# Performance work log

Measured on AMD Instinct MI355X. Metric: run time of the kernel, lower is better.

The kernel has to match this reference:

```python
import math
import jax, jax.numpy as jnp
import numpy as np

FACTOR = 5

def setup_inputs() -> dict:
    key = jax.random.key(0)
    kq, kk, kv, ki = jax.random.split(key, 4)
    b, h, L, d = 4, 8, 4096, 64
    sample_k = min(L, int(FACTOR * math.log(L + 1)))  # 41
    q = jax.random.normal(kq, (b, h, L, d), dtype=jnp.float32)
    k = jax.random.normal(kk, (b, h, L, d), dtype=jnp.float32)
    v = jax.random.normal(kv, (b, h, L, d), dtype=jnp.float32)
    index_sample = jax.random.randint(ki, (L, sample_k), 0, L, dtype=jnp.int64)
    return {"q": q, "k": k, "v": v, "index_sample": index_sample}

def reference(q, k, v, index_sample):
    b, h, l_q, d = q.shape
    l_k = k.shape[2]
    n_top = min(l_q, int(FACTOR * math.log(l_q + 1)))
    # --- ProbSparse query selection ---
    # k_sample[b,h,q,s,d] = k[b,h,index_sample[q,s],d]  (avoids the O(lq*lk*d) expand)
    k_sample = k[:, :, index_sample, :]                      # (b,h,l_q,sample_k,d)
    qk_sample = jnp.einsum('bhqd,bhqsd->bhqs', q, k_sample)  # (b,h,l_q,sample_k)
    m = qk_sample.max(axis=-1) - qk_sample.mean(axis=-1)     # sparsity measure
    _, top_q = jax.lax.top_k(m, n_top)                       # (b,h,n_top)
    # --- sparse attention on selected queries ---
    q_reduce = jnp.take_along_axis(q, top_q[..., None], axis=2)  # (b,h,n_top,d)
    scale = 1.0 / math.sqrt(d)
    scores = jnp.einsum('bhnd,bhkd->bhnk', q_reduce, k) * scale
    attn = jax.nn.softmax(scores, axis=-1)
    context_top = jnp.einsum('bhnk,bhkd->bhnd', attn, v)
    # --- scatter into mean-initialized context (attn_mask is None path) ---
    context = jnp.broadcast_to(v.mean(axis=2, keepdims=True), (b, h, l_q, d))
    bi = jnp.arange(b)[:, None, None]
    hi = jnp.arange(h)[None, :, None]
    context = context.at[bi, hi, top_q].set(context_top)
    return context
```

## Files before the change

### kernel.cpp

```cpp
#include <hip/hip_runtime.h>
#include <hip/hip_bf16.h>


#define NTOP 41
#define NPAD 48
#define TILES 8
#define TL 512
#define CH 64
#define NCHUNK (TL / CH)
#define CAND_CAP 64

typedef __attribute__((ext_vector_type(8))) short bf16x8;
typedef __attribute__((ext_vector_type(4))) float f32x4;

__device__ __forceinline__ unsigned short f2bf(float f) {
    unsigned int x = __float_as_uint(f);
    unsigned int r = (x + 0x7FFFu + ((x >> 16) & 1u)) >> 16;
    return (unsigned short)r;
}
__device__ __forceinline__ unsigned int pack2(float lo, float hi) {
    return ((unsigned int)f2bf(hi) << 16) | f2bf(lo);
}

__global__ __launch_bounds__(256) void kA_scores(const float* __restrict__ q,
                                                 const float* __restrict__ k,
                                                 const int* __restrict__ idxs,
                                                 float* __restrict__ m_out) {
    int t = threadIdx.x;
    int lane = t & 63, w = t >> 6;
    int g = lane >> 3, sl = lane & 7;
    int lb = ((blockIdx.x & 7) << 9) + (blockIdx.x >> 3);
    long long qflat = (long long)lb * 32 + w * 8 + g;
    int bh = (int)(qflat >> 12);
    int qi = (int)(qflat & 4095);
    const float4* q4 = (const float4*)q;
    const float4* k4 = (const float4*)k;
    float4 qa = q4[qflat * 16 + sl * 2];
    float4 qb = q4[qflat * 16 + sl * 2 + 1];
    const int* irow = idxs + qi * 41;
    long long kbase = ((long long)bh << 12) * 16;
    float maxv = -1e30f, sum = 0.f;
    for (int s = 0; s < 41; s++) {
        int ki = irow[s] & 4095;
        float4 ka = k4[kbase + (long long)ki * 16 + sl * 2];
        float4 kb = k4[kbase + (long long)ki * 16 + sl * 2 + 1];
        float p = 0.f;
        p = fmaf(qa.x, ka.x, p); p = fmaf(qa.y, ka.y, p);
        p = fmaf(qa.z, ka.z, p); p = fmaf(qa.w, ka.w, p);
        p = fmaf(qb.x, kb.x, p); p = fmaf(qb.y, kb.y, p);
        p = fmaf(qb.z, kb.z, p); p = fmaf(qb.w, kb.w, p);
        p += __shfl_xor(p, 1);
        p += __shfl_xor(p, 2);
        p += __shfl_xor(p, 4);
        maxv = fmaxf(maxv, p);
        sum += p;
    }
    if (sl == 0) m_out[qflat] = maxv - sum * (1.0f / 41.0f);
}

__global__ __launch_bounds__(256) void kB_topk(const float* __restrict__ m_in,
                                               int* __restrict__ topq) {
    __shared__ unsigned int uvals[4096];
    __shared__ unsigned int hist[256];
    __shared__ unsigned int scal[4];
    __shared__ int candIdx[CAND_CAP];
    __shared__ unsigned int candU[CAND_CAP];
    int bh = blockIdx.x, t = threadIdx.x;
    for (int i = t; i < 4096; i += 256) {
        unsigned int b = __float_as_uint(m_in[bh * 4096 + i]);
        uvals[i] = (b & 0x80000000u) ? ~b : (b | 0x80000000u);
    }
    hist[t] = 0;
    __syncthreads();
    for (int i = t; i < 4096; i += 256) atomicAdd(&hist[uvals[i] >> 24], 1u);
    __syncthreads();
    if (t == 0) {
        unsigned int cum = 0, b1 = 0, ca = 0;
        for (int j = 255; j >= 0; j--) {
            if (cum + hist[j] >= 41u) { b1 = (unsigned)j; ca = cum; break; }
            cum += hist[j];
        }
        scal[0] = b1; scal[1] = ca;
    }
    __syncthreads();
    unsigned int b1 = scal[0];
    hist[t] = 0;
    __syncthreads();
    for (int i = t; i < 4096; i += 256)
        if ((uvals[i] >> 24) == b1) atomicAdd(&hist[(uvals[i] >> 16) & 255u], 1u);
    __syncthreads();
    if (t == 0) {
        unsigned int cum = scal[1], b2 = 0;
        for (int j = 255; j >= 0; j--) {
            if (cum + hist[j] >= 41u) { b2 = (unsigned)j; break; }
            cum += hist[j];
        }
        scal[2] = (b1 << 24) | (b2 << 16);
        scal[3] = 0;
    }
    __syncthreads();
    unsigned int T = scal[2];
    for (int i = t; i < 4096; i += 256) {
        unsigned int u = uvals[i];
        if (u >= T) {
            unsigned int pos = atomicAdd(&scal[3], 1u);
            if (pos < CAND_CAP) { candIdx[pos] = i; candU[pos] = u; }
        }
    }
    __syncthreads();
    if (t < 64) {
        int n = (int)min(scal[3], (unsigned)CAND_CAP);
        unsigned int myU = (t < n) ? candU[t] : 0u;
        int myI = (t < n) ? candIdx[t] : 0x7fffffff;
        for (int it = 0; it < NTOP; it++) {
            unsigned int bu = myU;
            int bi = myI;
            for (int off = 32; off; off >>= 1) {
                unsigned int ou = __shfl_xor(bu, off);
                int oi = __shfl_xor(bi, off);
                if (ou > bu || (ou == bu && oi < bi)) { bu = ou; bi = oi; }
            }
            if (t == 0) topq[bh * NTOP + it] = bi;
            if (myI == bi) { myU = 0u; myI = 0x7fffffff; }
        }
    }
}

__global__ __launch_bounds__(256) void kC1(const float* __restrict__ v,
                                           float* __restrict__ vpart) {
    int bh = blockIdx.x, chn = blockIdx.y, t = threadIdx.x;
    int d = t & 63, r = t >> 6;
    long long base = ((long long)bh << 12) + chn * 256;
    float acc = 0.f;
    for (int i = 0; i < 64; i++) acc += v[(base + i * 4 + r) * 64 + d];
    __shared__ float red[256];
    red[t] = acc;
    __syncthreads();
    if (r == 0) vpart[(bh * 16 + chn) * 64 + d] = red[d] + red[64 + d] + red[128 + d] + red[192 + d];
}

__global__ void kC2(const float* __restrict__ vpart, float* __restrict__ vmean) {
    int bh = blockIdx.x, d = threadIdx.x;
    float s = 0.f;
#pragma unroll
    for (int c = 0; c < 16; c++) s += vpart[(bh * 16 + c) * 64 + d];
    vmean[bh * 64 + d] = s * (1.0f / 4096.0f);
}

__global__ __launch_bounds__(256) void kD(const float* __restrict__ vmean,
                                          float* __restrict__ out) {
    long long g0 = (long long)blockIdx.x * 1024 + threadIdx.x;
    float4* out4 = (float4*)out;
#pragma unroll
    for (int i = 0; i < 4; i++) {
        long long g = g0 + i * 256;
        int bh = (int)(g >> 16);
        int d4 = (int)(g & 15);
        out4[g] = *(const float4*)(vmean + bh * 64 + d4 * 4);
    }
}

__global__ __launch_bounds__(256) void kE_attn(const float* __restrict__ q,
                                               const float* __restrict__ k,
                                               const float* __restrict__ v,
                                               const int* __restrict__ topq,
                                               float* __restrict__ part) {
    __shared__ unsigned short qs[NPAD * 72];
    __shared__ unsigned short kb[CH * 72];
    __shared__ unsigned short vt[64 * 72];
    __shared__ unsigned short pb[NPAD * 72];
    __shared__ float sp[NPAD * 65];
    __shared__ float m_i[NPAD], l_i[NPAD], fac[NPAD];

    const int t = threadIdx.x;
    const int tile = blockIdx.x, bh = blockIdx.y;
    const int lane = t & 63, w = t >> 6;
    const int c = lane & 15, quad = lane >> 4;
    const long long bhbase = ((long long)bh) << 12;

    const float4* q4f = (const float4*)q;
    const float4* k4f = (const float4*)k;
    const float4* v4f = (const float4*)v;

    for (int i = t; i < NTOP * 16; i += 256) {
        int n = i >> 4, oc = i & 15;
        int row = topq[bh * NTOP + n];
        float4 val = q4f[(bhbase + row) * 16 + oc];
        uint2 pk;
        pk.x = pack2(val.x * 0.125f, val.y * 0.125f);
        pk.y = pack2(val.z * 0.125f, val.w * 0.125f);
        *(uint2*)(&qs[n * 72 + oc * 4]) = pk;
    }
    for (int i = t; i < 7 * 72; i += 256) {
        qs[NTOP * 72 + i] = 0;
        pb[NTOP * 72 + i] = 0;
    }
    if (t < NPAD) { m_i[t] = -1e30f; l_i[t] = 0.f; fac[t] = 0.f; }

    f32x4 oacc[3];
#pragma unroll
    for (int qt = 0; qt < 3; qt++) oacc[qt] = (f32x4){0.f, 0.f, 0.f, 0.f};

    const int l0 = tile * TL;
    for (int ch = 0; ch < NCHUNK; ch++) {
        const int lb = l0 + ch * CH;
        __syncthreads();
#pragma unroll
        for (int i = 0; i < 4; i++) {
            int idx = i * 256 + t;
            int j = idx >> 4, oc = idx & 15;
            float4 val = k4f[(bhbase + lb + j) * 16 + oc];
            uint2 pk;
            pk.x = pack2(val.x, val.y);
            pk.y = pack2(val.z, val.w);
            *(uint2*)(&kb[j * 72 + oc * 4]) = pk;
        }
        {
            int jp = t & 31, o = t >> 5;
            float4 a0 = v4f[(bhbase + lb + 2 * jp) * 16 + o * 2];
            float4 a1 = v4f[(bhbase + lb + 2 * jp) * 16 + o * 2 + 1];
            float4 b0 = v4f[(bhbase + lb + 2 * jp + 1) * 16 + o * 2];
            float4 b1 = v4f[(bhbase + lb + 2 * jp + 1) * 16 + o * 2 + 1];
            float av[8] = {a0.x, a0.y, a0.z, a0.w, a1.x, a1.y, a1.z, a1.w};
            float bv[8] = {b0.x, b0.y, b0.z, b0.w, b1.x, b1.y, b1.z, b1.w};
#pragma unroll
            for (int e = 0; e < 8; e++)
                *(unsigned int*)(&vt[(o * 8 + e) * 72 + 2 * jp]) = pack2(av[e], bv[e]);
        }
        __syncthreads();
        {
            const bf16x8 bk0 = *(const bf16x8*)(&kb[(w * 16 + c) * 72 + quad * 8]);
            const bf16x8 bk1 = *(const bf16x8*)(&kb[(w * 16 + c) * 72 + quad * 8 + 32]);
#pragma unroll
            for (int qt = 0; qt < 3; qt++) {
                const bf16x8 a0 = *(const bf16x8*)(&qs[(qt * 16 + c) * 72 + quad * 8]);
                const bf16x8 a1 = *(const bf16x8*)(&qs[(qt * 16 + c) * 72 + quad * 8 + 32]);
                f32x4 s4 = (f32x4){0.f, 0.f, 0.f, 0.f};
                s4 = __builtin_amdgcn_mfma_f32_16x16x32_bf16(a0, bk0, s4, 0, 0, 0);
                s4 = __builtin_amdgcn_mfma_f32_16x16x32_bf16(a1, bk1, s4, 0, 0, 0);
#pragma unroll
                for (int r = 0; r < 4; r++)
                    sp[(qt * 16 + quad * 4 + r) * 65 + w * 16 + c] = s4[r];
            }
        }
        __syncthreads();
        if (t < NTOP * 4) {
            int n = t >> 2, sub = t & 3;
            float rm = -1e30f;
#pragma unroll
            for (int j = 0; j < 16; j++) rm = fmaxf(rm, sp[n * 65 + sub * 16 + j]);
            rm = fmaxf(rm, __shfl_xor(rm, 1));
            rm = fmaxf(rm, __shfl_xor(rm, 2));
            float mo = m_i[n];
            float mn = fmaxf(mo, rm);
            float ssum = 0.f;
#pragma unroll
            for (int j = 0; j < 16; j += 2) {
                float e0 = __expf(sp[n * 65 + sub * 16 + j] - mn);
                float e1 = __expf(sp[n * 65 + sub * 16 + j + 1] - mn);
                ssum += e0 + e1;
                *(unsigned int*)(&pb[n * 72 + sub * 16 + j]) = pack2(e0, e1);
            }
            ssum += __shfl_xor(ssum, 1);
            ssum += __shfl_xor(ssum, 2);
            if (sub == 0) {
                float f = __expf(mo - mn);
                fac[n] = f;
                l_i[n] = l_i[n] * f + ssum;
                m_i[n] = mn;
            }
        }
        __syncthreads();
        {
            const bf16x8 bv0 = *(const bf16x8*)(&vt[(w * 16 + c) * 72 + quad * 8]);
            const bf16x8 bv1 = *(const bf16x8*)(&vt[(w * 16 + c) * 72 + quad * 8 + 32]);
#pragma unroll
            for (int qt = 0; qt < 3; qt++) {
                const bf16x8 a0 = *(const bf16x8*)(&pb[(qt * 16 + c) * 72 + quad * 8]);
                const bf16x8 a1 = *(const bf16x8*)(&pb[(qt * 16 + c) * 72 + quad * 8 + 32]);
                f32x4 o = oacc[qt];
                o.x *= fac[qt * 16 + quad * 4 + 0];
                o.y *= fac[qt * 16 + quad * 4 + 1];
                o.z *= fac[qt * 16 + quad * 4 + 2];
                o.w *= fac[qt * 16 + quad * 4 + 3];
                o = __builtin_amdgcn_mfma_f32_16x16x32_bf16(a0, bv0, o, 0, 0, 0);
                o = __builtin_amdgcn_mfma_f32_16x16x32_bf16(a1, bv1, o, 0, 0, 0);
                oacc[qt] = o;
            }
        }
    }
    __syncthreads();
    long long pbase = ((long long)(bh * TILES + tile)) * NTOP * 66;
    if (t < NTOP) {
        part[pbase + t * 66 + 0] = m_i[t];
        part[pbase + t * 66 + 1] = l_i[t];
    }
#pragma unroll
    for (int qt = 0; qt < 3; qt++) {
#pragma unroll
        for (int r = 0; r < 4; r++) {
            int n = qt * 16 + quad * 4 + r;
            if (n < NTOP) part[pbase + (long long)n * 66 + 2 + w * 16 + c] = oacc[qt][r];
        }
    }
}

__global__ __launch_bounds__(256) void kF_combine(const float* __restrict__ part,
                                                  const int* __restrict__ topq,
                                                  float* __restrict__ out) {
    int t = threadIdx.x;
    int bh = blockIdx.x;
    int n = blockIdx.y * 4 + (t >> 6);
    int d = t & 63;
    if (n >= NTOP) return;
    long long base = ((long long)(bh * TILES)) * NTOP * 66 + (long long)n * 66;
    const long long ts = (long long)NTOP * 66;
    float M = -1e30f;
#pragma unroll
    for (int tt = 0; tt < TILES; tt++) M = fmaxf(M, part[base + tt * ts]);
    float L = 0.f, acc = 0.f;
#pragma unroll
    for (int tt = 0; tt < TILES; tt++) {
        float mt = part[base + tt * ts];
        float wgt = __expf(mt - M);
        L += part[base + tt * ts + 1] * wgt;
        acc += part[base + tt * ts + 2 + d] * wgt;
    }
    int row = topq[bh * NTOP + n];
    out[(((long long)bh << 12) + row) * 64 + d] = acc / L;
}

extern "C" void kernel_launch(void* const* d_in, const int* in_sizes, int n_in,
                              void* d_out, int out_size, void* d_ws, size_t ws_size,
                              hipStream_t stream) {
    const float* q = (const float*)d_in[0];
    const float* k = (const float*)d_in[1];
    const float* v = (const float*)d_in[2];
    const int* idxs = (const int*)d_in[3];
    float* out = (float*)d_out;

    char* ws = (char*)d_ws;
    float* ws_m = (float*)ws;
    int* ws_topq = (int*)(ws + 524288);
    float* ws_vpart = (float*)(ws + 532480);
    float* ws_vmean = (float*)(ws + 663552);
    float* ws_part = (float*)(ws + 671744);

    kA_scores<<<4096, 256, 0, stream>>>(q, k, idxs, ws_m);
    kB_topk<<<32, 256, 0, stream>>>(ws_m, ws_topq);
    kC1<<<dim3(32, 16), 256, 0, stream>>>(v, ws_vpart);
    kC2<<<32, 64, 0, stream>>>(ws_vpart, ws_vmean);
    kD<<<2048, 256, 0, stream>>>(ws_vmean, out);
    kE_attn<<<dim3(TILES, 32), 256, 0, stream>>>(q, k, v, ws_topq, ws_part);
    kF_combine<<<dim3(32, 11), 256, 0, stream>>>(ws_part, ws_topq, out);
}
```

Measured before the change: 261.6 us.

## Stage sample indices in LDS, fold vmean into fill, split attention into more tiles

New measurement: 252.1 us. 1.04x faster.

```diff
diff --git a/kernel.cpp b/kernel.cpp
--- a/kernel.cpp
+++ b/kernel.cpp
@@ -4,10 +4,7 @@
 
 #define NTOP 41
 #define NPAD 48
-#define TILES 8
-#define TL 512
 #define CH 64
-#define NCHUNK (TL / CH)
 #define CAND_CAP 64
 
 typedef __attribute__((ext_vector_type(8))) short bf16x8;
@@ -21,37 +18,68 @@
 __device__ __forceinline__ unsigned int pack2(float lo, float hi) {
     return ((unsigned int)f2bf(hi) << 16) | f2bf(lo);
 }
+__device__ __forceinline__ float dot8(const float4& qa, const float4& qb,
+                                      const float4& ka, const float4& kb) {
+    float p = 0.f;
+    p = fmaf(qa.x, ka.x, p); p = fmaf(qa.y, ka.y, p);
+    p = fmaf(qa.z, ka.z, p); p = fmaf(qa.w, ka.w, p);
+    p = fmaf(qb.x, kb.x, p); p = fmaf(qb.y, kb.y, p);
+    p = fmaf(qb.z, kb.z, p); p = fmaf(qb.w, kb.w, p);
+    return p;
+}
+__device__ __forceinline__ float red8(float p) {
+    p += __shfl_xor(p, 1);
+    p += __shfl_xor(p, 2);
+    p += __shfl_xor(p, 4);
+    return p;
+}
 
 __global__ __launch_bounds__(256) void kA_scores(const float* __restrict__ q,
                                                  const float* __restrict__ k,
                                                  const int* __restrict__ idxs,
                                                  float* __restrict__ m_out) {
+    __shared__ int sidx[32 * 41];
     int t = threadIdx.x;
     int lane = t & 63, w = t >> 6;
     int g = lane >> 3, sl = lane & 7;
     int lb = ((blockIdx.x & 7) << 9) + (blockIdx.x >> 3);
     long long qflat = (long long)lb * 32 + w * 8 + g;
     int bh = (int)(qflat >> 12);
-    int qi = (int)(qflat & 4095);
+    int qi0 = (lb * 32) & 4095;
+    for (int i = t; i < 32 * 41; i += 256)
+        sidx[i] = idxs[(long long)qi0 * 41 + i] & 4095;
     const float4* q4 = (const float4*)q;
     const float4* k4 = (const float4*)k;
     float4 qa = q4[qflat * 16 + sl * 2];
     float4 qb = q4[qflat * 16 + sl * 2 + 1];
-    const int* irow = idxs + qi * 41;
     long long kbase = ((long long)bh << 12) * 16;
+    __syncthreads();
+    const int* irow = sidx + (w * 8 + g) * 41;
     float maxv = -1e30f, sum = 0.f;
-    for (int s = 0; s < 41; s++) {
-        int ki = irow[s] & 4095;
+#pragma unroll 2
+    for (int g4 = 0; g4 < 10; g4++) {
+        int ki0 = irow[g4 * 4 + 0], ki1 = irow[g4 * 4 + 1];
+        int ki2 = irow[g4 * 4 + 2], ki3 = irow[g4 * 4 + 3];
+        float4 ka0 = k4[kbase + (long long)ki0 * 16 + sl * 2];
+        float4 kb0 = k4[kbase + (long long)ki0 * 16 + sl * 2 + 1];
+        float4 ka1 = k4[kbase + (long long)ki1 * 16 + sl * 2];
+        float4 kb1 = k4[kbase + (long long)ki1 * 16 + sl * 2 + 1];
+        float4 ka2 = k4[kbase + (long long)ki2 * 16 + sl * 2];
+        float4 kb2 = k4[kbase + (long long)ki2 * 16 + sl * 2 + 1];
+        float4 ka3 = k4[kbase + (long long)ki3 * 16 + sl * 2];
+        float4 kb3 = k4[kbase + (long long)ki3 * 16 + sl * 2 + 1];
+        float p0 = red8(dot8(qa, qb, ka0, kb0));
+        float p1 = red8(dot8(qa, qb, ka1, kb1));
+        float p2 = red8(dot8(qa, qb, ka2, kb2));
+        float p3 = red8(dot8(qa, qb, ka3, kb3));
+        maxv = fmaxf(maxv, fmaxf(fmaxf(p0, p1), fmaxf(p2, p3)));
+        sum += (p0 + p1) + (p2 + p3);
+    }
+    {
+        int ki = irow[40];
         float4 ka = k4[kbase + (long long)ki * 16 + sl * 2];
         float4 kb = k4[kbase + (long long)ki * 16 + sl * 2 + 1];
-        float p = 0.f;
-        p = fmaf(qa.x, ka.x, p); p = fmaf(qa.y, ka.y, p);
-        p = fmaf(qa.z, ka.z, p); p = fmaf(qa.w, ka.w, p);
-        p = fmaf(qb.x, kb.x, p); p = fmaf(qb.y, kb.y, p);
-        p = fmaf(qb.z, kb.z, p); p = fmaf(qb.w, kb.w, p);
-        p += __shfl_xor(p, 1);
-        p += __shfl_xor(p, 2);
-        p += __shfl_xor(p, 4);
+        float p = red8(dot8(qa, qb, ka, kb));
         maxv = fmaxf(maxv, p);
         sum += p;
     }
@@ -139,24 +167,25 @@
     if (r == 0) vpart[(bh * 16 + chn) * 64 + d] = red[d] + red[64 + d] + red[128 + d] + red[192 + d];
 }
 
-__global__ void kC2(const float* __restrict__ vpart, float* __restrict__ vmean) {
-    int bh = blockIdx.x, d = threadIdx.x;
-    float s = 0.f;
-#pragma unroll
-    for (int c = 0; c < 16; c++) s += vpart[(bh * 16 + c) * 64 + d];
-    vmean[bh * 64 + d] = s * (1.0f / 4096.0f);
-}
-
-__global__ __launch_bounds__(256) void kD(const float* __restrict__ vmean,
+__global__ __launch_bounds__(256) void kD(const float* __restrict__ vpart,
                                           float* __restrict__ out) {
-    long long g0 = (long long)blockIdx.x * 1024 + threadIdx.x;
+    __shared__ __align__(16) float vm[64];
+    int t = threadIdx.x;
+    int bh = blockIdx.x >> 6;
+    if (t < 64) {
+        float s = 0.f;
+#pragma unroll
+        for (int c = 0; c < 16; c++) s += vpart[(bh * 16 + c) * 64 + t];
+        vm[t] = s * (1.0f / 4096.0f);
+    }
+    __syncthreads();
+    long long g0 = (long long)blockIdx.x * 1024 + t;
     float4* out4 = (float4*)out;
 #pragma unroll
     for (int i = 0; i < 4; i++) {
-        long long g = g0 + i * 256;
-        int bh = (int)(g >> 16);
-        int d4 = (int)(g & 15);
-        out4[g] = *(const float4*)(vmean + bh * 64 + d4 * 4);
+        long long gg = g0 + i * 256;
+        int d4 = (int)(gg & 15);
+        out4[gg] = *(const float4*)(&vm[d4 * 4]);
     }
 }
 
@@ -164,7 +193,7 @@
                                                const float* __restrict__ k,
                                                const float* __restrict__ v,
                                                const int* __restrict__ topq,
-                                               float* __restrict__ part) {
+                                               float* __restrict__ part, int tl) {
     __shared__ unsigned short qs[NPAD * 72];
     __shared__ unsigned short kb[CH * 72];
     __shared__ unsigned short vt[64 * 72];
@@ -174,6 +203,7 @@
 
     const int t = threadIdx.x;
     const int tile = blockIdx.x, bh = blockIdx.y;
+    const int tiles = gridDim.x;
     const int lane = t & 63, w = t >> 6;
     const int c = lane & 15, quad = lane >> 4;
     const long long bhbase = ((long long)bh) << 12;
@@ -201,8 +231,9 @@
 #pragma unroll
     for (int qt = 0; qt < 3; qt++) oacc[qt] = (f32x4){0.f, 0.f, 0.f, 0.f};
 
-    const int l0 = tile * TL;
-    for (int ch = 0; ch < NCHUNK; ch++) {
+    const int l0 = tile * tl;
+    const int nchunk = tl >> 6;
+    for (int ch = 0; ch < nchunk; ch++) {
         const int lb = l0 + ch * CH;
         __syncthreads();
 #pragma unroll
@@ -290,7 +321,7 @@
         }
     }
     __syncthreads();
-    long long pbase = ((long long)(bh * TILES + tile)) * NTOP * 66;
+    long long pbase = ((long long)(bh * tiles + tile)) * NTOP * 66;
     if (t < NTOP) {
         part[pbase + t * 66 + 0] = m_i[t];
         part[pbase + t * 66 + 1] = l_i[t];
@@ -307,20 +338,18 @@
 
 __global__ __launch_bounds__(256) void kF_combine(const float* __restrict__ part,
                                                   const int* __restrict__ topq,
-                                                  float* __restrict__ out) {
+                                                  float* __restrict__ out, int tiles) {
     int t = threadIdx.x;
     int bh = blockIdx.x;
     int n = blockIdx.y * 4 + (t >> 6);
     int d = t & 63;
     if (n >= NTOP) return;
-    long long base = ((long long)(bh * TILES)) * NTOP * 66 + (long long)n * 66;
+    long long base = ((long long)(bh * tiles)) * NTOP * 66 + (long long)n * 66;
     const long long ts = (long long)NTOP * 66;
     float M = -1e30f;
-#pragma unroll
-    for (int tt = 0; tt < TILES; tt++) M = fmaxf(M, part[base + tt * ts]);
+    for (int tt = 0; tt < tiles; tt++) M = fmaxf(M, part[base + tt * ts]);
     float L = 0.f, acc = 0.f;
-#pragma unroll
-    for (int tt = 0; tt < TILES; tt++) {
+    for (int tt = 0; tt < tiles; tt++) {
         float mt = part[base + tt * ts];
         float wgt = __expf(mt - M);
         L += part[base + tt * ts + 1] * wgt;
@@ -343,14 +372,16 @@
     float* ws_m = (float*)ws;
     int* ws_topq = (int*)(ws + 524288);
     float* ws_vpart = (float*)(ws + 532480);
-    float* ws_vmean = (float*)(ws + 663552);
     float* ws_part = (float*)(ws + 671744);
+
+    size_t need16 = 671744ull + 16ull * 32 * NTOP * 66 * 4;
+    int tiles = (ws_size >= need16) ? 16 : 8;
+    int tl = 4096 / tiles;
 
     kA_scores<<<4096, 256, 0, stream>>>(q, k, idxs, ws_m);
     kB_topk<<<32, 256, 0, stream>>>(ws_m, ws_topq);
     kC1<<<dim3(32, 16), 256, 0, stream>>>(v, ws_vpart);
-    kC2<<<32, 64, 0, stream>>>(ws_vpart, ws_vmean);
-    kD<<<2048, 256, 0, stream>>>(ws_vmean, out);
-    kE_attn<<<dim3(TILES, 32), 256, 0, stream>>>(q, k, v, ws_topq, ws_part);
-    kF_combine<<<dim3(32, 11), 256, 0, stream>>>(ws_part, ws_topq, out);
-}
+    kD<<<2048, 256, 0, stream>>>(ws_vpart, out);
+    kE_attn<<<dim3(tiles, 32), 256, 0, stream>>>(q, k, v, ws_topq, ws_part, tl);
+    kF_combine<<<dim3(32, 11), 256, 0, stream>>>(ws_part, ws_topq, out, tiles);
+}
```
